# Kernel optimization log

Measured on AMD Instinct MI355X. Metric: run time of the kernel, lower is better.

Reference implementation:

```python
import jax, jax.numpy as jnp
import numpy as np

ALPHA = 1.0
RANK = 4


def _conv2d_same(x, w):
    # x: [B,C,H,W], w: [O,C,kh,kw], stride 1, 'same' padding
    return jax.lax.conv_general_dilated(
        x, w, window_strides=(1, 1), padding='SAME',
        dimension_numbers=('NCHW', 'OIHW', 'NCHW'))


def setup_inputs() -> dict:
    key = jax.random.key(0)
    k1, k2, k3, k4, k5 = jax.random.split(key, 5)
    B, C, H, W = 32, 64, 64, 256
    O, E, r, k = 64, 4, RANK, 3
    x = jax.random.normal(k1, (B, C, H, W), dtype=jnp.float32)
    subject_id = jax.random.randint(k2, (B,), 0, E, dtype=jnp.int64)
    W_conv = jax.random.normal(k3, (O, C, k, k), dtype=jnp.float32) * (1.0 / np.sqrt(C * k * k))
    W_A = jax.random.normal(k4, (E, r, C, k, k), dtype=jnp.float32) * 0.02
    # torch init zeros W_B; use random here so the LoRA path is numerically exercised
    W_B = jax.random.normal(k5, (E, O, r), dtype=jnp.float32) * 0.02
    return {'x': x, 'subject_id': subject_id, 'W_conv': W_conv, 'W_A': W_A, 'W_B': W_B}


def reference(x, subject_id, W_conv, W_A, W_B):
    B, C, H, W = x.shape
    E, r = W_A.shape[0], W_A.shape[1]
    k = W_A.shape[-1]
    # Base conv
    out = _conv2d_same(x, W_conv)  # [B,O,H,W]
    # Run all adapter A-convs in one batched conv (E*r tiny output channels),
    # then per-sample select the adapter matching subject_id (same math as the
    # masked per-adapter dispatch in the original).
    a_all = _conv2d_same(x, W_A.reshape(E * r, C, k, k))  # [B,E*r,H,W]
    a_all = a_all.reshape(B, E, r, H, W)
    idx = subject_id[:, None, None, None, None]
    a_sel = jnp.take_along_axis(a_all, idx, axis=1)[:, 0]  # [B,r,H,W]
    wb_sel = W_B[subject_id]  # [B,O,r] (1x1 conv weight per sample)
    lora = (ALPHA / r) * jnp.einsum('bor,brhw->bohw', wb_sel, a_sel)
    return out + lora
```

## Files before the change

### kernel.cpp

```cpp
#include <hip/hip_runtime.h>
#include <hip/hip_bf16.h>

typedef __attribute__((ext_vector_type(8)))  short bf16x8;
typedef __attribute__((ext_vector_type(16))) float f32x16;

constexpr int Bn = 32, Cn = 64, Hn = 64, Wn = 256, On = 64, En = 4, Rn = 4;
constexpr float SCALE = 1.0f / Rn;

constexpr int WTILE  = 64;
constexpr int HSTRIP = 8;
constexpr int SLOT_B = 66 * 128;

__device__ __forceinline__ int swz(int ww, int cb) {
    return ww * 128 + ((cb ^ ((ww >> 2) & 7)) * 16);
}

__global__ __launch_bounds__(256) void merge_k(
    const float* __restrict__ Wc, const float* __restrict__ Wa,
    const float* __restrict__ Wb, __hip_bfloat16* __restrict__ Wfrag)
{
    int t = blockIdx.x * 256 + threadIdx.x;
    int j    = t & 7;
    int lane = (t >> 3) & 63;
    int g    = t >> 9;
    int s    = g % 36;
    int mh   = (g / 36) & 1;
    int e    = g / 72;
    int m = lane & 31, half = lane >> 5;
    int o = mh * 32 + m;
    int tap = s >> 2, cq = s & 3;
    int c = cq * 16 + half * 8 + j;
    float acc = Wc[(o * Cn + c) * 9 + tap];
#pragma unroll
    for (int r = 0; r < Rn; ++r)
        acc += SCALE * Wb[(e * On + o) * Rn + r] * Wa[((e * Rn + r) * Cn + c) * 9 + tap];
    Wfrag[t] = __float2bfloat16(acc);
}

__global__ __launch_bounds__(128, 2) void conv6_k(
    const float* __restrict__ x, const int* __restrict__ sid,
    const __hip_bfloat16* __restrict__ Wfrag, float* __restrict__ out)
{
    __shared__ __align__(16) char xs[4 * SLOT_B];

    const int tid = threadIdx.x;
    const int w0  = blockIdx.x * WTILE;
    const int h0  = blockIdx.y * HSTRIP;
    const int b   = blockIdx.z;
    const int e   = sid[b];
    const size_t HW = (size_t)Hn * Wn;

    const int lane = tid & 63, wave = tid >> 6;
    const int mh = wave;
    const int n = lane & 31, half = lane >> 5;

    bf16x8 wf[36];
    const bf16x8* wg = reinterpret_cast<const bf16x8*>(Wfrag) + (size_t)(e * 2 + mh) * 36 * 64;
#pragma unroll
    for (int s = 0; s < 36; ++s) wf[s] = wg[s * 64 + lane];

    const int cb = tid >> 4;
    const int q  = tid & 15;
    const float* xbase = x + ((size_t)b * Cn + cb * 8) * HW + w0 + 4 * q;

    const int hside = tid >> 4;
    const int hidx  = tid & 15;
    const int hcb   = hidx >> 1, hhi = hidx & 1;
    const int gwh   = hside ? (w0 + WTILE) : (w0 - 1);
    const bool hv   = (unsigned)gwh < (unsigned)Wn;
    const float* hbase = x + ((size_t)b * Cn + hcb * 8 + hhi * 4) * HW + gwh;

    float4 f[8];
    float  hx[4];

    auto stage_load = [&](int rx) {
        const int gh = h0 + rx;
        if ((unsigned)gh < (unsigned)Hn) {
            const float* src = xbase + (size_t)gh * Wn;
#pragma unroll
            for (int r = 0; r < 8; ++r)
                f[r] = *reinterpret_cast<const float4*>(src + r * HW);
            if (tid < 32) {
                if (hv) {
                    const float* hs = hbase + (size_t)gh * Wn;
#pragma unroll
                    for (int i = 0; i < 4; ++i) hx[i] = hs[i * HW];
                } else {
#pragma unroll
                    for (int i = 0; i < 4; ++i) hx[i] = 0.0f;
                }
            }
        } else {
            float4 z4 = make_float4(0.0f, 0.0f, 0.0f, 0.0f);
#pragma unroll
            for (int r = 0; r < 8; ++r) f[r] = z4;
#pragma unroll
            for (int i = 0; i < 4; ++i) hx[i] = 0.0f;
        }
    };
    auto stage_store = [&](int rx) {
        const int slot = (rx + 1) & 3;
        char* dbase = xs + slot * SLOT_B;
#pragma unroll
        for (int j = 0; j < 4; ++j) {
            union { __hip_bfloat16 u[8]; bf16x8 v; } pk;
#pragma unroll
            for (int r = 0; r < 8; ++r) {
                float v = (j == 0) ? f[r].x : (j == 1) ? f[r].y : (j == 2) ? f[r].z : f[r].w;
                pk.u[r] = __float2bfloat16(v);
            }
            int ww = 4 * q + 1 + j;
            *reinterpret_cast<bf16x8*>(dbase + swz(ww, cb)) = pk.v;
        }
        if (tid < 32) {
            union { __hip_bfloat16 u[4]; short4 v; } pk;
#pragma unroll
            for (int i = 0; i < 4; ++i) pk.u[i] = __float2bfloat16(hx[i]);
            int ww = hside ? (WTILE + 1) : 0;
            *reinterpret_cast<short4*>(dbase + swz(ww, hcb) + hhi * 8) = pk.v;
        }
    };

    auto barrier = [&]() {
        asm volatile("s_waitcnt lgkmcnt(0)" ::: "memory");
        __builtin_amdgcn_s_barrier();
    };

    stage_load(-1); stage_store(-1);
    stage_load(0);  stage_store(0);
    stage_load(1);  stage_store(1);
    barrier();

    for (int st = 0; st < HSTRIP; ++st) {
        const bool do_stage = (st + 2 <= HSTRIP);
        if (do_stage) stage_load(st + 2);

        f32x16 a[2];
#pragma unroll
        for (int nf = 0; nf < 2; ++nf)
#pragma unroll
            for (int i = 0; i < 16; ++i) a[nf][i] = 0.0f;

#pragma unroll
        for (int s = 0; s < 36; ++s) {
            const int tap = s >> 2, cq = s & 3;
            const int dh = tap / 3, dw = tap % 3;
            const int slotbase = ((st + dh) & 3) * SLOT_B;
#pragma unroll
            for (int nf = 0; nf < 2; ++nf) {
                int ww = nf * 32 + n + dw;
                bf16x8 bf = *reinterpret_cast<const bf16x8*>(xs + slotbase + swz(ww, cq * 2 + half));
                a[nf] = __builtin_amdgcn_mfma_f32_32x32x16_bf16(wf[s], bf, a[nf], 0, 0, 0);
            }
        }

        if (do_stage) stage_store(st + 2);

        {
            const int hrow = h0 + st;
            size_t base = ((size_t)(b * On + mh * 32 + 4 * half) * Hn + hrow) * Wn
                          + w0 + n;
#pragma unroll
            for (int nf = 0; nf < 2; ++nf)
#pragma unroll
                for (int r = 0; r < 16; ++r) {
                    int o_off = (r & 3) + 8 * (r >> 2);
                    out[base + (size_t)o_off * HW + nf * 32] = a[nf][r];
                }
        }

        barrier();
    }
}

extern "C" void kernel_launch(void* const* d_in, const int* in_sizes, int n_in,
                              void* d_out, int out_size, void* d_ws, size_t ws_size,
                              hipStream_t stream)
{
    const float* x   = (const float*)d_in[0];
    const int*   sid = (const int*)d_in[1];
    const float* Wc  = (const float*)d_in[2];
    const float* Wa  = (const float*)d_in[3];
    const float* Wb  = (const float*)d_in[4];
    float*       out = (float*)d_out;

    __hip_bfloat16* Wfrag = (__hip_bfloat16*)d_ws;

    merge_k<<<En * 2 * 36 * 64 * 8 / 256, 256, 0, stream>>>(Wc, Wa, Wb, Wfrag);

    dim3 grid(Wn / WTILE, Hn / HSTRIP, Bn);
    conv6_k<<<grid, 128, 0, stream>>>(x, sid, Wfrag, out);
}
```

Baseline: 274.3 us.

## Narrow conv tile to 32 columns, taller strip, double-buffered register prefetch

Halves the width tile to 32 and doubles the row strip to 16. Each wave now runs one 32x32 MFMA chain per row instead of two. Global loads are issued two rows ahead into alternating register buffers, which deepens prefetch beyond the previous one-row lookahead. Halo loading is spread across all threads as scalar loads. The cost is fewer independent MFMA accumulators per wave, which exposes more MFMA latency, and lower LDS reuse per halo column.

```diff
diff --git a/kernel.cpp b/kernel.cpp
--- a/kernel.cpp
+++ b/kernel.cpp
@@ -7,9 +7,9 @@
 constexpr int Bn = 32, Cn = 64, Hn = 64, Wn = 256, On = 64, En = 4, Rn = 4;
 constexpr float SCALE = 1.0f / Rn;
 
-constexpr int WTILE  = 64;
-constexpr int HSTRIP = 8;
-constexpr int SLOT_B = 66 * 128;
+constexpr int WTILE  = 32;
+constexpr int HSTRIP = 16;
+constexpr int SLOT_B = 34 * 128;
 
 __device__ __forceinline__ int swz(int ww, int cb) {
     return ww * 128 + ((cb ^ ((ww >> 2) & 7)) * 16);
@@ -37,7 +37,7 @@
     Wfrag[t] = __float2bfloat16(acc);
 }
 
-__global__ __launch_bounds__(128, 2) void conv6_k(
+__global__ __launch_bounds__(128, 2) void conv8_k(
     const float* __restrict__ x, const int* __restrict__ sid,
     const __hip_bfloat16* __restrict__ Wfrag, float* __restrict__ out)
 {
@@ -50,8 +50,7 @@
     const int e   = sid[b];
     const size_t HW = (size_t)Hn * Wn;
 
-    const int lane = tid & 63, wave = tid >> 6;
-    const int mh = wave;
+    const int lane = tid & 63, mh = tid >> 6;
     const int n = lane & 31, half = lane >> 5;
 
     bf16x8 wf[36];
@@ -59,65 +58,48 @@
 #pragma unroll
     for (int s = 0; s < 36; ++s) wf[s] = wg[s * 64 + lane];
 
-    const int cb = tid >> 4;
-    const int q  = tid & 15;
-    const float* xbase = x + ((size_t)b * Cn + cb * 8) * HW + w0 + 4 * q;
+    const int pb = tid >> 3, q = tid & 7;
+    const float* xbase = x + ((size_t)b * Cn + pb * 4) * HW + w0 + 4 * q;
 
-    const int hside = tid >> 4;
-    const int hidx  = tid & 15;
-    const int hcb   = hidx >> 1, hhi = hidx & 1;
+    const int hside = tid >> 6, hc = tid & 63;
     const int gwh   = hside ? (w0 + WTILE) : (w0 - 1);
     const bool hv   = (unsigned)gwh < (unsigned)Wn;
-    const float* hbase = x + ((size_t)b * Cn + hcb * 8 + hhi * 4) * HW + gwh;
+    const float* hbase = x + ((size_t)b * Cn + hc) * HW + gwh;
 
-    float4 f[8];
-    float  hx[4];
-
-    auto stage_load = [&](int rx) {
+    auto stage_load = [&](float4 (&f)[4], float& hx, int rx) {
         const int gh = h0 + rx;
         if ((unsigned)gh < (unsigned)Hn) {
             const float* src = xbase + (size_t)gh * Wn;
 #pragma unroll
-            for (int r = 0; r < 8; ++r)
+            for (int r = 0; r < 4; ++r)
                 f[r] = *reinterpret_cast<const float4*>(src + r * HW);
-            if (tid < 32) {
-                if (hv) {
-                    const float* hs = hbase + (size_t)gh * Wn;
-#pragma unroll
-                    for (int i = 0; i < 4; ++i) hx[i] = hs[i * HW];
-                } else {
-#pragma unroll
-                    for (int i = 0; i < 4; ++i) hx[i] = 0.0f;
-                }
-            }
+            hx = hv ? hbase[(size_t)gh * Wn] : 0.0f;
         } else {
             float4 z4 = make_float4(0.0f, 0.0f, 0.0f, 0.0f);
 #pragma unroll
-            for (int r = 0; r < 8; ++r) f[r] = z4;
-#pragma unroll
-            for (int i = 0; i < 4; ++i) hx[i] = 0.0f;
+            for (int r = 0; r < 4; ++r) f[r] = z4;
+            hx = 0.0f;
         }
     };
-    auto stage_store = [&](int rx) {
+    auto stage_store = [&](float4 (&f)[4], float& hx, int rx) {
         const int slot = (rx + 1) & 3;
         char* dbase = xs + slot * SLOT_B;
+        const int cb = pb >> 1, sub = (pb & 1) * 8;
 #pragma unroll
         for (int j = 0; j < 4; ++j) {
-            union { __hip_bfloat16 u[8]; bf16x8 v; } pk;
+            union { __hip_bfloat16 u[4]; short4 v; } pk;
 #pragma unroll
-            for (int r = 0; r < 8; ++r) {
+            for (int r = 0; r < 4; ++r) {
                 float v = (j == 0) ? f[r].x : (j == 1) ? f[r].y : (j == 2) ? f[r].z : f[r].w;
                 pk.u[r] = __float2bfloat16(v);
             }
             int ww = 4 * q + 1 + j;
-            *reinterpret_cast<bf16x8*>(dbase + swz(ww, cb)) = pk.v;
+            *reinterpret_cast<short4*>(dbase + swz(ww, cb) + sub) = pk.v;
         }
-        if (tid < 32) {
-            union { __hip_bfloat16 u[4]; short4 v; } pk;
-#pragma unroll
-            for (int i = 0; i < 4; ++i) pk.u[i] = __float2bfloat16(hx[i]);
+        {
+            __hip_bfloat16 hb = __float2bfloat16(hx);
             int ww = hside ? (WTILE + 1) : 0;
-            *reinterpret_cast<short4*>(dbase + swz(ww, hcb) + hhi * 8) = pk.v;
+            *reinterpret_cast<__hip_bfloat16*>(dbase + swz(ww, hc >> 3) + (hc & 7) * 2) = hb;
         }
     };
 
@@ -126,47 +108,50 @@
         __builtin_amdgcn_s_barrier();
     };
 
-    stage_load(-1); stage_store(-1);
-    stage_load(0);  stage_store(0);
-    stage_load(1);  stage_store(1);
+    float4 fA[4], fB[4];
+    float  hxA, hxB;
+
+    stage_load(fA, hxA, -1); stage_store(fA, hxA, -1);
+    stage_load(fA, hxA, 0);  stage_store(fA, hxA, 0);
+    stage_load(fA, hxA, 1);  stage_store(fA, hxA, 1);
+    stage_load(fA, hxA, 2);
     barrier();
 
     for (int st = 0; st < HSTRIP; ++st) {
-        const bool do_stage = (st + 2 <= HSTRIP);
-        if (do_stage) stage_load(st + 2);
+        const bool do_issue = (st + 3 <= HSTRIP);
+        if (do_issue) {
+            if (st & 1) stage_load(fA, hxA, st + 3);
+            else        stage_load(fB, hxB, st + 3);
+        }
 
-        f32x16 a[2];
+        f32x16 a;
 #pragma unroll
-        for (int nf = 0; nf < 2; ++nf)
-#pragma unroll
-            for (int i = 0; i < 16; ++i) a[nf][i] = 0.0f;
+        for (int i = 0; i < 16; ++i) a[i] = 0.0f;
 
 #pragma unroll
         for (int s = 0; s < 36; ++s) {
             const int tap = s >> 2, cq = s & 3;
             const int dh = tap / 3, dw = tap % 3;
             const int slotbase = ((st + dh) & 3) * SLOT_B;
-#pragma unroll
-            for (int nf = 0; nf < 2; ++nf) {
-                int ww = nf * 32 + n + dw;
-                bf16x8 bf = *reinterpret_cast<const bf16x8*>(xs + slotbase + swz(ww, cq * 2 + half));
-                a[nf] = __builtin_amdgcn_mfma_f32_32x32x16_bf16(wf[s], bf, a[nf], 0, 0, 0);
-            }
+            int ww = n + dw;
+            bf16x8 bf = *reinterpret_cast<const bf16x8*>(xs + slotbase + swz(ww, cq * 2 + half));
+            a = __builtin_amdgcn_mfma_f32_32x32x16_bf16(wf[s], bf, a, 0, 0, 0);
         }
 
-        if (do_stage) stage_store(st + 2);
+        const bool do_store = (st + 2 <= HSTRIP);
+        if (do_store) {
+            if (st & 1) stage_store(fB, hxB, st + 2);
+            else        stage_store(fA, hxA, st + 2);
+        }
 
         {
             const int hrow = h0 + st;
-            size_t base = ((size_t)(b * On + mh * 32 + 4 * half) * Hn + hrow) * Wn
-                          + w0 + n;
+            size_t base = ((size_t)(b * On + mh * 32 + 4 * half) * Hn + hrow) * Wn + w0 + n;
 #pragma unroll
-            for (int nf = 0; nf < 2; ++nf)
-#pragma unroll
-                for (int r = 0; r < 16; ++r) {
-                    int o_off = (r & 3) + 8 * (r >> 2);
-                    out[base + (size_t)o_off * HW + nf * 32] = a[nf][r];
-                }
+            for (int r = 0; r < 16; ++r) {
+                int o_off = (r & 3) + 8 * (r >> 2);
+                out[base + (size_t)o_off * HW] = a[r];
+            }
         }
 
         barrier();
@@ -189,5 +174,5 @@
     merge_k<<<En * 2 * 36 * 64 * 8 / 256, 256, 0, stream>>>(Wc, Wa, Wb, Wfrag);
 
     dim3 grid(Wn / WTILE, Hn / HSTRIP, Bn);
-    conv6_k<<<grid, 128, 0, stream>>>(x, sid, Wfrag, out);
+    conv8_k<<<grid, 128, 0, stream>>>(x, sid, Wfrag, out);
 }
```

New measurement: 273.5 us. Within noise of the previous version (-0.3%).
